# Kernel optimization log

Measured on AMD Instinct MI355X. Metric: run time of the kernel, lower is better.

Reference implementation:

```python
import jax, jax.numpy as jnp
import numpy as np

B, NPG, IN_DIM, HID, H, DEG, NTYPE, NLAYERS = 4, 5000, 16, 128, 8, 32, 12, 4
N = B * NPG
DH = HID // H
E = N * DEG + N  # random edges + self loops


def setup_inputs() -> dict:
    key = jax.random.key(0)
    ks = jax.random.split(key, 10)
    e_rand = N * DEG
    # intra-graph random edges: sample within [0, NPG) then offset by graph id
    src = jax.random.randint(ks[0], (e_rand,), 0, NPG, dtype=jnp.int32)
    dst = jax.random.randint(ks[1], (e_rand,), 0, NPG, dtype=jnp.int32)
    gid = jnp.repeat(jnp.arange(B, dtype=jnp.int32), NPG * DEG) * NPG
    loops = jnp.arange(N, dtype=jnp.int32)
    edge_index = jnp.stack([jnp.concatenate([src + gid, loops]),
                            jnp.concatenate([dst + gid, loops])])
    edge_type = jnp.concatenate([
        jax.random.randint(ks[2], (e_rand,), 1, NTYPE, dtype=jnp.int32),
        jnp.zeros((N,), jnp.int32)])  # self-loop type = 0
    feat = jax.random.normal(ks[3], (N, IN_DIM), jnp.float32)
    s = 0.1
    return {
        "feat": feat,
        "edge_table": jax.random.normal(ks[4], (NTYPE, HID), jnp.float32) * s,
        "W_embed": jax.random.normal(ks[5], (IN_DIM, HID), jnp.float32) * s,
        "b_embed": jnp.zeros((HID,), jnp.float32),
        "W_conv": jax.random.normal(ks[6], (HID, HID), jnp.float32) * s,
        "a_src": jax.random.normal(ks[7], (H, DH), jnp.float32) * s,
        "a_dst": jax.random.normal(ks[8], (H, DH), jnp.float32) * s,
        "a_edge": jax.random.normal(ks[9], (H, DH), jnp.float32) * s,
        "edge_index": edge_index,
        "edge_type": edge_type,
    }


def _forward(feat, edge_table, W_embed, b_embed, W_conv, a_src, a_dst, a_edge,
             edge_index, edge_type):
    src, dst = edge_index[0], edge_index[1]
    # feature masking done in the torch forward
    feat = feat.at[:, 2:4].set(0.0).at[:, 10:].set(0.0)
    # 'sum'-flavor edge embedding: type lookup -> [E, H, DH]
    e_feat = edge_table[edge_type].reshape(-1, H, DH)
    ea = jnp.sum(e_feat * a_edge, axis=-1)  # [E, H]
    h = jax.nn.gelu(feat @ W_embed + b_embed)  # node embedder MLP
    layers = [feat, h]
    for _ in range(NLAYERS):  # shared_conv=True: same weights each layer
        z = (h @ W_conv).reshape(N, H, DH)
        s_logit = jnp.sum(z * a_src, axis=-1)  # [N, H]
        d_logit = jnp.sum(z * a_dst, axis=-1)
        logit = jax.nn.leaky_relu(s_logit[src] + d_logit[dst] + ea, 0.2)
        # numerically-stable edge softmax over incoming edges of each dst
        m = jax.ops.segment_max(logit, dst, num_segments=N)
        ex = jnp.exp(logit - jax.lax.stop_gradient(m)[dst])
        denom = jax.ops.segment_sum(ex, dst, num_segments=N)
        alpha = ex / (denom[dst] + 1e-9)  # [E, H]
        msg = alpha[..., None] * z[src]  # [E, H, DH]
        agg = jax.ops.segment_sum(msg, dst, num_segments=N).reshape(N, HID)
        h = h + jax.nn.gelu(agg)  # residual
        layers.append(h)
    feats_all = jnp.concatenate(layers, axis=1)  # layer_pooling='all' -> [N, 656]
    nf = feats_all.reshape(B, NPG, -1)
    g_emb = jnp.max(nf, axis=1, keepdims=True)  # graph_pooling='max'
    return jnp.concatenate([nf, jnp.broadcast_to(g_emb, nf.shape)], axis=2)


def reference(feat, edge_table, W_embed, b_embed, W_conv, a_src, a_dst, a_edge,
              edge_index, edge_type):
    return _forward(feat, edge_table, W_embed, b_embed, W_conv, a_src, a_dst,
                    a_edge, edge_index, edge_type)
```

## Files before the change

kernel.cpp:

```cpp
#include <hip/hip_runtime.h>
#include <math.h>

#define IN_DIM 16
#define HIDN 128
#define NH 8
#define DHD 16
#define NTYPE 12
#define NLAYERS 4
#define NPG 5000
#define NSEGP 250
#define RPS (NPG / NSEGP)
#define C1 656
#define C2 1312
#define C1Q (C1 / 4)
#define CAP 64
#define NPW 4
#define HREG (NPG / 2)
#define GEMM_SLOTS ((HREG + 63) / 64)
#define EDGE_SLOTS (HREG / NPW)

__device__ __forceinline__ float gelu_t(float x) {
    float x3 = x * x * x;
    float u = 0.7978845608028654f * (x + 0.044715f * x3);
    return 0.5f * x * (1.0f + tanhf(u));
}

__device__ __forceinline__ unsigned pack_bf16(float lo, float hi) {
    unsigned a = __float_as_uint(lo);
    unsigned b = __float_as_uint(hi);
    a = (a + 0x7fffu + ((a >> 16) & 1u)) >> 16;
    b = (b + 0x7fffu + ((b >> 16) & 1u)) & 0xffff0000u;
    return a | b;
}

__device__ __forceinline__ float lrelu(float x) { return (x >= 0.f) ? x : 0.2f * x; }

__global__ __launch_bounds__(256) void k_init(const float* __restrict__ etab,
                                              const float* __restrict__ aed,
                                              float* __restrict__ ea, int* __restrict__ cnt,
                                              int N) {
    int i = blockIdx.x * 256 + threadIdx.x;
    if (i < NTYPE * NH) {
        int t = i / NH, hh = i % NH;
        float s = 0.f;
        #pragma unroll
        for (int d = 0; d < DHD; d++) s += etab[t * HIDN + hh * DHD + d] * aed[hh * DHD + d];
        ea[i] = s;
    }
    if (i < N) cnt[i] = 0;
}

__global__ __launch_bounds__(128) void k_embed(const float* __restrict__ feat,
                                               const float* __restrict__ We,
                                               const float* __restrict__ be,
                                               float* __restrict__ h, float* __restrict__ out,
                                               int N) {
    int n = blockIdx.x;
    int c = threadIdx.x;
    __shared__ float f[IN_DIM];
    if (c < IN_DIM) {
        float v = feat[n * IN_DIM + c];
        if ((c >= 2 && c < 4) || c >= 10) v = 0.f;
        f[c] = v;
        out[(size_t)n * C2 + c] = v;
    }
    __syncthreads();
    float a = be[c];
    #pragma unroll
    for (int k = 0; k < IN_DIM; k++) a += f[k] * We[k * HIDN + c];
    float g = gelu_t(a);
    h[(size_t)n * HIDN + c] = g;
    out[(size_t)n * C2 + IN_DIM + c] = g;
}

__global__ void k_bucket(const int* __restrict__ srcp, const int* __restrict__ dstp,
                         const int* __restrict__ etp, int* __restrict__ cnt,
                         unsigned* __restrict__ payload2, int E) {
    int e = blockIdx.x * 256 + threadIdx.x;
    if (e < E) {
        int d = dstp[e];
        int slot = atomicAdd(&cnt[d], 1);
        if (slot < CAP)
            payload2[(size_t)d * CAP + slot] = (unsigned)srcp[e] | ((unsigned)etp[e] << 16);
    }
}

#define KC 64
__global__ __launch_bounds__(256) void k_gemm(const float* __restrict__ h,
                                              const float* __restrict__ W,
                                              const float* __restrict__ asf,
                                              const float* __restrict__ adf,
                                              unsigned* __restrict__ z16,
                                              float* __restrict__ slog,
                                              float* __restrict__ dlog, int N) {
    __shared__ float Wc[KC][HIDN];
    __shared__ float hc[64][KC + 4];
    int xcd = blockIdx.x & 7, slot = blockIdx.x >> 3;
    int g = xcd & 3, half = xcd >> 2;
    int base = g * NPG + half * HREG;
    int rend = base + HREG;
    int n0 = base + slot * 64;
    int t = threadIdx.x;
    int cg = t & 15, rg = t >> 4;
    int c0 = cg * 8;
    float acc[4][8];
    #pragma unroll
    for (int i = 0; i < 4; i++)
        #pragma unroll
        for (int j = 0; j < 8; j++) acc[i][j] = 0.f;

    for (int k0 = 0; k0 < HIDN; k0 += KC) {
        for (int i = t; i < KC * 32; i += 256) {
            int kk = i >> 5, cc = (i & 31) << 2;
            *(float4*)&Wc[kk][cc] = *(const float4*)&W[(k0 + kk) * HIDN + cc];
        }
        for (int i = t; i < 64 * (KC / 4); i += 256) {
            int rr = i / (KC / 4), kk = (i % (KC / 4)) * 4;
            int n = n0 + rr;
            float4 v = make_float4(0.f, 0.f, 0.f, 0.f);
            if (n < rend) v = *(const float4*)&h[(size_t)n * HIDN + k0 + kk];
            *(float4*)&hc[rr][kk] = v;
        }
        __syncthreads();
        for (int k = 0; k < KC; k++) {
            float4 w0 = *(float4*)&Wc[k][c0];
            float4 w1 = *(float4*)&Wc[k][c0 + 4];
            float hv[4];
            #pragma unroll
            for (int i = 0; i < 4; i++) hv[i] = hc[rg + 16 * i][k];
            #pragma unroll
            for (int i = 0; i < 4; i++) {
                acc[i][0] += hv[i] * w0.x;
                acc[i][1] += hv[i] * w0.y;
                acc[i][2] += hv[i] * w0.z;
                acc[i][3] += hv[i] * w0.w;
                acc[i][4] += hv[i] * w1.x;
                acc[i][5] += hv[i] * w1.y;
                acc[i][6] += hv[i] * w1.z;
                acc[i][7] += hv[i] * w1.w;
            }
        }
        __syncthreads();
    }
    float4 s0 = *(const float4*)&asf[c0];
    float4 s1 = *(const float4*)&asf[c0 + 4];
    float4 d0 = *(const float4*)&adf[c0];
    float4 d1 = *(const float4*)&adf[c0 + 4];
    #pragma unroll
    for (int i = 0; i < 4; i++) {
        int n = n0 + rg + 16 * i;
        float ps = acc[i][0] * s0.x + acc[i][1] * s0.y + acc[i][2] * s0.z + acc[i][3] * s0.w +
                   acc[i][4] * s1.x + acc[i][5] * s1.y + acc[i][6] * s1.z + acc[i][7] * s1.w;
        float pd = acc[i][0] * d0.x + acc[i][1] * d0.y + acc[i][2] * d0.z + acc[i][3] * d0.w +
                   acc[i][4] * d1.x + acc[i][5] * d1.y + acc[i][6] * d1.z + acc[i][7] * d1.w;
        ps += __shfl_xor(ps, 1);
        pd += __shfl_xor(pd, 1);
        unsigned u[8];
        #pragma unroll
        for (int j = 0; j < 8; j++) {
            float other = __shfl_xor(acc[i][j], 8);
            u[j] = pack_bf16(acc[i][j], other);
        }
        if (n < rend) {
            if (cg < 8) {
                *(uint4*)&z16[(size_t)n * 64 + c0] = make_uint4(u[0], u[1], u[2], u[3]);
                *(uint4*)&z16[(size_t)n * 64 + c0 + 4] = make_uint4(u[4], u[5], u[6], u[7]);
            }
            if ((cg & 1) == 0) {
                slog[n * NH + (cg >> 1)] = ps;
                dlog[n * NH + (cg >> 1)] = pd;
            }
        }
    }
}

__global__ __launch_bounds__(256) void k_edge(const int* __restrict__ cnt,
                                              const unsigned* __restrict__ payload2,
                                              const float* __restrict__ slog,
                                              const float* __restrict__ dlog,
                                              const float* __restrict__ ea,
                                              const unsigned* __restrict__ z16,
                                              float* __restrict__ h,
                                              float* __restrict__ out, int colbase, int N) {
    int wave = threadIdx.x >> 6, lane = threadIdx.x & 63;
    int xcd = blockIdx.x & 7, slot = blockIdx.x >> 3;
    int g = xcd & 3, half = xcd >> 2;
    int unit = g * (NPG / NPW) + half * EDGE_SLOTS + slot;
    int n = unit * NPW + wave;
    bool active = (n < N);
    __shared__ float lbuf[NPW][CAP * NH];
    __shared__ unsigned pbuf[NPW][CAP];
    __shared__ float dl[NPW][NH];
    __shared__ float red[NPW][NH];
    __shared__ float sea[NTYPE * NH];

    if (threadIdx.x < NTYPE * NH) sea[threadIdx.x] = ea[threadIdx.x];

    int cntE = 0;
    if (active) {
        cntE = cnt[n];
        if (cntE > CAP) cntE = CAP;
        if (lane < NH) dl[wave][lane] = dlog[n * NH + lane];
    }
    if (lane < cntE) pbuf[wave][lane] = payload2[(size_t)n * CAP + lane];
    __syncthreads();

    int o = lane & 1;
    int eoff = lane >> 1;
    float4 dl4 = *(float4*)&dl[wave][o * 4];
    float4 ssum4 = make_float4(0.f, 0.f, 0.f, 0.f);
    #pragma unroll
    for (int base = 0; base < CAP; base += 32) {
        int el = base + eoff;
        if (el < cntE) {
            unsigned pk = pbuf[wave][el];
            int src = pk & 0xffff;
            int et = pk >> 16;
            float4 s4 = *(const float4*)&slog[src * NH + o * 4];
            float4 e4 = *(float4*)&sea[et * NH + o * 4];
            float4 ex;
            ex.x = __expf(lrelu(s4.x + dl4.x + e4.x));
            ex.y = __expf(lrelu(s4.y + dl4.y + e4.y));
            ex.z = __expf(lrelu(s4.z + dl4.z + e4.z));
            ex.w = __expf(lrelu(s4.w + dl4.w + e4.w));
            *(float4*)&lbuf[wave][el * NH + o * 4] = ex;
            ssum4.x += ex.x;
            ssum4.y += ex.y;
            ssum4.z += ex.z;
            ssum4.w += ex.w;
        }
    }
    #pragma unroll
    for (int m = 2; m <= 32; m <<= 1) {
        ssum4.x += __shfl_xor(ssum4.x, m);
        ssum4.y += __shfl_xor(ssum4.y, m);
        ssum4.z += __shfl_xor(ssum4.z, m);
        ssum4.w += __shfl_xor(ssum4.w, m);
    }
    if (lane < 2) {
        float4 r4;
        r4.x = 1.0f / (ssum4.x + 1e-9f);
        r4.y = 1.0f / (ssum4.y + 1e-9f);
        r4.z = 1.0f / (ssum4.z + 1e-9f);
        r4.w = 1.0f / (ssum4.w + 1e-9f);
        *(float4*)&red[wave][o * 4] = r4;
    }
    __syncthreads();

    int h1 = lane >> 4, h2 = h1 + 4;
    float r1 = red[wave][h1], r2 = red[wave][h2];
    float a0 = 0.f, a1 = 0.f;
    int e = 0;
    for (; e + 7 < cntE; e += 8) {
        unsigned v[8];
        #pragma unroll
        for (int j = 0; j < 8; j++) {
            unsigned s = pbuf[wave][e + j] & 0xffff;
            v[j] = z16[(size_t)s * 64 + lane];
        }
        #pragma unroll
        for (int j = 0; j < 8; j++) {
            float l0 = lbuf[wave][(e + j) * NH + h1];
            float l1 = lbuf[wave][(e + j) * NH + h2];
            a0 += l0 * __uint_as_float(v[j] << 16);
            a1 += l1 * __uint_as_float(v[j] & 0xffff0000u);
        }
    }
    for (; e < cntE; e++) {
        unsigned s0 = pbuf[wave][e] & 0xffff;
        unsigned v0 = z16[(size_t)s0 * 64 + lane];
        a0 += lbuf[wave][e * NH + h1] * __uint_as_float(v0 << 16);
        a1 += lbuf[wave][e * NH + h2] * __uint_as_float(v0 & 0xffff0000u);
    }
    if (active) {
        a0 *= r1;
        a1 *= r2;
        size_t hb = (size_t)n * HIDN;
        float o0 = h[hb + lane] + gelu_t(a0);
        float o1 = h[hb + lane + 64] + gelu_t(a1);
        h[hb + lane] = o0;
        h[hb + lane + 64] = o1;
        size_t ob = (size_t)n * C2 + colbase;
        out[ob + lane] = o0;
        out[ob + lane + 64] = o1;
    }
}

__global__ __launch_bounds__(256) void k_pool_partial(const float* __restrict__ out,
                                                      float* __restrict__ gpart) {
    int b = blockIdx.x / NSEGP, seg = blockIdx.x % NSEGP;
    int n0 = b * NPG + seg * RPS;
    for (int c = threadIdx.x; c < C1; c += 256) {
        float m = -3.4e38f;
        #pragma unroll
        for (int i = 0; i < RPS; i++) m = fmaxf(m, out[(size_t)(n0 + i) * C2 + c]);
        gpart[(size_t)(b * NSEGP + seg) * C1 + c] = m;
    }
}

__global__ __launch_bounds__(256) void k_pool_final(const float* __restrict__ gpart,
                                                    float* __restrict__ gemb, int B) {
    int w = blockIdx.x * 4 + (threadIdx.x >> 6);
    int lane = threadIdx.x & 63;
    if (w >= B * C1) return;
    int b = w / C1, c = w % C1;
    float m = -3.4e38f;
    for (int s = lane; s < NSEGP; s += 64) m = fmaxf(m, gpart[(size_t)(b * NSEGP + s) * C1 + c]);
    #pragma unroll
    for (int k = 1; k < 64; k <<= 1) m = fmaxf(m, __shfl_xor(m, k));
    if (lane == 0) gemb[w] = m;
}

__global__ __launch_bounds__(256) void k_bcast(const float* __restrict__ gemb,
                                               float* __restrict__ out, int N) {
    int idx = blockIdx.x * 256 + threadIdx.x;
    if (idx < N * C1Q) {
        int n = idx / C1Q, c4 = idx % C1Q;
        int b = n / NPG;
        float4 g = *(const float4*)&gemb[b * C1 + c4 * 4];
        *(float4*)&out[(size_t)n * C2 + C1 + c4 * 4] = g;
    }
}

extern "C" void kernel_launch(void* const* d_in, const int* in_sizes, int n_in, void* d_out,
                              int out_size, void* d_ws, size_t ws_size, hipStream_t stream) {
    const float* feat = (const float*)d_in[0];
    const float* etab = (const float*)d_in[1];
    const float* We = (const float*)d_in[2];
    const float* be = (const float*)d_in[3];
    const float* Wc = (const float*)d_in[4];
    const float* a_src = (const float*)d_in[5];
    const float* a_dst = (const float*)d_in[6];
    const float* a_edge = (const float*)d_in[7];
    const int* eidx = (const int*)d_in[8];
    const int* etype = (const int*)d_in[9];
    float* out = (float*)d_out;

    const int N = in_sizes[0] / IN_DIM;
    const int E = in_sizes[9];
    const int B = N / NPG;

    const int* srcp = eidx;
    const int* dstp = eidx + E;

    char* w = (char*)d_ws;
    size_t off = 0;
    auto carve = [&](size_t bytes) {
        char* p = w + off;
        off = (off + bytes + 255) & ~(size_t)255;
        return p;
    };
    float* h = (float*)carve((size_t)N * HIDN * 4);
    unsigned* z16 = (unsigned*)carve((size_t)N * 64 * 4);
    float* slog = (float*)carve((size_t)N * NH * 4);
    float* dlog = (float*)carve((size_t)N * NH * 4);
    float* ea = (float*)carve(NTYPE * NH * 4);
    int* cnt = (int*)carve((size_t)N * 4);
    unsigned* payload2 = (unsigned*)carve((size_t)N * CAP * 4);
    float* gpart = (float*)carve((size_t)B * NSEGP * C1 * 4);
    float* gemb = (float*)carve((size_t)B * C1 * 4);
    (void)ws_size;

    k_init<<<(N + 255) / 256, 256, 0, stream>>>(etab, a_edge, ea, cnt, N);
    k_embed<<<N, 128, 0, stream>>>(feat, We, be, h, out, N);
    k_bucket<<<(E + 255) / 256, 256, 0, stream>>>(srcp, dstp, etype, cnt, payload2, E);

    for (int l = 0; l < NLAYERS; l++) {
        k_gemm<<<8 * GEMM_SLOTS, 256, 0, stream>>>(h, Wc, a_src, a_dst, z16, slog, dlog, N);
        int colbase = IN_DIM + HIDN * (l + 1);
        k_edge<<<8 * EDGE_SLOTS, 256, 0, stream>>>(cnt, payload2, slog, dlog, ea, z16,
                                                   h, out, colbase, N);
    }

    k_pool_partial<<<B * NSEGP, 256, 0, stream>>>(out, gpart);
    k_pool_final<<<(B * C1 + 3) / 4, 256, 0, stream>>>(gpart, gemb, B);
    k_bcast<<<((size_t)N * C1Q + 255) / 256, 256, 0, stream>>>(gemb, out, N);
}
```

Baseline: 253.8 us.

## Drop separate h buffer, fuse embed with bucketing, XCD-aware pooling

Removes the standalone h workspace so that the GEMM and edge kernels read the previous layer straight from the output tensor's strided columns and write the new layer only there, avoiding the duplicate h store. The embed and edge-bucketing kernels merge into one launch, with the embed using wave shuffles instead of shared memory plus a barrier. The GEMM weight tile in shared memory is split into two halves to change the access pattern. Pool-partial blocks are remapped so each XCD handles one graph half for L2 locality. The trade-off is that h is now read with a large stride (C2) instead of from a contiguous array.

```diff
diff --git a/kernel.cpp b/kernel.cpp
--- a/kernel.cpp
+++ b/kernel.cpp
@@ -50,34 +50,37 @@
     if (i < N) cnt[i] = 0;
 }
 
-__global__ __launch_bounds__(128) void k_embed(const float* __restrict__ feat,
-                                               const float* __restrict__ We,
-                                               const float* __restrict__ be,
-                                               float* __restrict__ h, float* __restrict__ out,
-                                               int N) {
-    int n = blockIdx.x;
-    int c = threadIdx.x;
-    __shared__ float f[IN_DIM];
-    if (c < IN_DIM) {
-        float v = feat[n * IN_DIM + c];
-        if ((c >= 2 && c < 4) || c >= 10) v = 0.f;
-        f[c] = v;
-        out[(size_t)n * C2 + c] = v;
-    }
-    __syncthreads();
-    float a = be[c];
-    #pragma unroll
-    for (int k = 0; k < IN_DIM; k++) a += f[k] * We[k * HIDN + c];
-    float g = gelu_t(a);
-    h[(size_t)n * HIDN + c] = g;
-    out[(size_t)n * C2 + IN_DIM + c] = g;
-}
-
-__global__ void k_bucket(const int* __restrict__ srcp, const int* __restrict__ dstp,
-                         const int* __restrict__ etp, int* __restrict__ cnt,
-                         unsigned* __restrict__ payload2, int E) {
-    int e = blockIdx.x * 256 + threadIdx.x;
-    if (e < E) {
+__global__ __launch_bounds__(256) void k_pre(const float* __restrict__ feat,
+                                             const float* __restrict__ We,
+                                             const float* __restrict__ be,
+                                             const int* __restrict__ srcp,
+                                             const int* __restrict__ dstp,
+                                             const int* __restrict__ etp,
+                                             int* __restrict__ cnt,
+                                             unsigned* __restrict__ payload2,
+                                             float* __restrict__ out, int N, int E) {
+    int bid = blockIdx.x, tid = threadIdx.x;
+    int wave = tid >> 6, lane = tid & 63;
+    int n = bid * NPW + wave;
+    if (n < N) {
+        float v = 0.f;
+        if (lane < IN_DIM) {
+            v = feat[n * IN_DIM + lane];
+            if ((lane >= 2 && lane < 4) || lane >= 10) v = 0.f;
+            out[(size_t)n * C2 + lane] = v;
+        }
+        float a0 = be[lane], a1 = be[lane + 64];
+        #pragma unroll
+        for (int k = 0; k < IN_DIM; k++) {
+            float fk = __shfl(v, k);
+            a0 += fk * We[k * HIDN + lane];
+            a1 += fk * We[k * HIDN + lane + 64];
+        }
+        size_t ob = (size_t)n * C2 + IN_DIM;
+        out[ob + lane] = gelu_t(a0);
+        out[ob + lane + 64] = gelu_t(a1);
+    }
+    for (int e = bid * 256 + tid; e < E; e += gridDim.x * 256) {
         int d = dstp[e];
         int slot = atomicAdd(&cnt[d], 1);
         if (slot < CAP)
@@ -86,14 +89,15 @@
 }
 
 #define KC 64
-__global__ __launch_bounds__(256) void k_gemm(const float* __restrict__ h,
+__global__ __launch_bounds__(256) void k_gemm(const float* __restrict__ out,
                                               const float* __restrict__ W,
                                               const float* __restrict__ asf,
                                               const float* __restrict__ adf,
                                               unsigned* __restrict__ z16,
                                               float* __restrict__ slog,
-                                              float* __restrict__ dlog, int N) {
-    __shared__ float Wc[KC][HIDN];
+                                              float* __restrict__ dlog, int prevbase, int N) {
+    __shared__ float WcA[KC][64];
+    __shared__ float WcB[KC][64];
     __shared__ float hc[64][KC + 4];
     int xcd = blockIdx.x & 7, slot = blockIdx.x >> 3;
     int g = xcd & 3, half = xcd >> 2;
@@ -103,6 +107,7 @@
     int t = threadIdx.x;
     int cg = t & 15, rg = t >> 4;
     int c0 = cg * 8;
+    const float* hin = out + prevbase;
     float acc[4][8];
     #pragma unroll
     for (int i = 0; i < 4; i++)
@@ -112,19 +117,22 @@
     for (int k0 = 0; k0 < HIDN; k0 += KC) {
         for (int i = t; i < KC * 32; i += 256) {
             int kk = i >> 5, cc = (i & 31) << 2;
-            *(float4*)&Wc[kk][cc] = *(const float4*)&W[(k0 + kk) * HIDN + cc];
+            float4 v = *(const float4*)&W[(k0 + kk) * HIDN + cc];
+            int halfcol = (cc & ~4) >> 1;
+            if (cc & 4) *(float4*)&WcB[kk][halfcol] = v;
+            else *(float4*)&WcA[kk][halfcol] = v;
         }
         for (int i = t; i < 64 * (KC / 4); i += 256) {
             int rr = i / (KC / 4), kk = (i % (KC / 4)) * 4;
             int n = n0 + rr;
             float4 v = make_float4(0.f, 0.f, 0.f, 0.f);
-            if (n < rend) v = *(const float4*)&h[(size_t)n * HIDN + k0 + kk];
+            if (n < rend) v = *(const float4*)&hin[(size_t)n * C2 + k0 + kk];
             *(float4*)&hc[rr][kk] = v;
         }
         __syncthreads();
         for (int k = 0; k < KC; k++) {
-            float4 w0 = *(float4*)&Wc[k][c0];
-            float4 w1 = *(float4*)&Wc[k][c0 + 4];
+            float4 w0 = *(float4*)&WcA[k][cg * 4];
+            float4 w1 = *(float4*)&WcB[k][cg * 4];
             float hv[4];
             #pragma unroll
             for (int i = 0; i < 4; i++) hv[i] = hc[rg + 16 * i][k];
@@ -180,8 +188,8 @@
                                               const float* __restrict__ dlog,
                                               const float* __restrict__ ea,
                                               const unsigned* __restrict__ z16,
-                                              float* __restrict__ h,
-                                              float* __restrict__ out, int colbase, int N) {
+                                              float* __restrict__ out, int prevbase,
+                                              int curbase, int N) {
     int wave = threadIdx.x >> 6, lane = threadIdx.x & 63;
     int xcd = blockIdx.x & 7, slot = blockIdx.x >> 3;
     int g = xcd & 3, half = xcd >> 2;
@@ -275,20 +283,19 @@
     if (active) {
         a0 *= r1;
         a1 *= r2;
-        size_t hb = (size_t)n * HIDN;
-        float o0 = h[hb + lane] + gelu_t(a0);
-        float o1 = h[hb + lane + 64] + gelu_t(a1);
-        h[hb + lane] = o0;
-        h[hb + lane + 64] = o1;
-        size_t ob = (size_t)n * C2 + colbase;
-        out[ob + lane] = o0;
-        out[ob + lane + 64] = o1;
+        size_t rowb = (size_t)n * C2;
+        float o0 = out[rowb + prevbase + lane] + gelu_t(a0);
+        float o1 = out[rowb + prevbase + lane + 64] + gelu_t(a1);
+        out[rowb + curbase + lane] = o0;
+        out[rowb + curbase + lane + 64] = o1;
     }
 }
 
 __global__ __launch_bounds__(256) void k_pool_partial(const float* __restrict__ out,
                                                       float* __restrict__ gpart) {
-    int b = blockIdx.x / NSEGP, seg = blockIdx.x % NSEGP;
+    int xcd = blockIdx.x & 7, slot = blockIdx.x >> 3;
+    int b = xcd & 3, half = xcd >> 2;
+    int seg = half * (NSEGP / 2) + slot;
     int n0 = b * NPG + seg * RPS;
     for (int c = threadIdx.x; c < C1; c += 256) {
         float m = -3.4e38f;
@@ -350,7 +357,6 @@
         off = (off + bytes + 255) & ~(size_t)255;
         return p;
     };
-    float* h = (float*)carve((size_t)N * HIDN * 4);
     unsigned* z16 = (unsigned*)carve((size_t)N * 64 * 4);
     float* slog = (float*)carve((size_t)N * NH * 4);
     float* dlog = (float*)carve((size_t)N * NH * 4);
@@ -362,17 +368,19 @@
     (void)ws_size;
 
     k_init<<<(N + 255) / 256, 256, 0, stream>>>(etab, a_edge, ea, cnt, N);
-    k_embed<<<N, 128, 0, stream>>>(feat, We, be, h, out, N);
-    k_bucket<<<(E + 255) / 256, 256, 0, stream>>>(srcp, dstp, etype, cnt, payload2, E);
+    k_pre<<<(N + NPW - 1) / NPW, 256, 0, stream>>>(feat, We, be, srcp, dstp, etype, cnt,
+                                                   payload2, out, N, E);
 
     for (int l = 0; l < NLAYERS; l++) {
-        k_gemm<<<8 * GEMM_SLOTS, 256, 0, stream>>>(h, Wc, a_src, a_dst, z16, slog, dlog, N);
-        int colbase = IN_DIM + HIDN * (l + 1);
-        k_edge<<<8 * EDGE_SLOTS, 256, 0, stream>>>(cnt, payload2, slog, dlog, ea, z16,
-                                                   h, out, colbase, N);
-    }
-
-    k_pool_partial<<<B * NSEGP, 256, 0, stream>>>(out, gpart);
+        int prevbase = IN_DIM + HIDN * l;
+        int curbase = IN_DIM + HIDN * (l + 1);
+        k_gemm<<<8 * GEMM_SLOTS, 256, 0, stream>>>(out, Wc, a_src, a_dst, z16, slog, dlog,
+                                                   prevbase, N);
+        k_edge<<<8 * EDGE_SLOTS, 256, 0, stream>>>(cnt, payload2, slog, dlog, ea, z16, out,
+                                                   prevbase, curbase, N);
+    }
+
+    k_pool_partial<<<8 * (NSEGP / 2), 256, 0, stream>>>(out, gpart);
     k_pool_final<<<(B * C1 + 3) / 4, 256, 0, stream>>>(gpart, gemb, B);
     k_bcast<<<((size_t)N * C1Q + 255) / 256, 256, 0, stream>>>(gemb, out, N);
 }
```

New measurement: 251.5 us, median of 2. No clear change (-0.9%).
